# Kernel tuning notes

Hardware: AMD Instinct MI355X
Metric: run time of the kernel (lower is better)

The kernel has to match this reference:

```python
import jax, jax.numpy as jnp
import numpy as np

# dims
B, N, T, F, D = 16, 64, 168, 8, 248   # batch, stations, seq, features, gcn_dim
E = D + F                              # transformer dmodel = 256
H = 8                                  # attention heads
FF = 4 * E                             # expansion_factor * dmodel


def _layer_norm(x, g, b, eps=1e-5):
    m = jnp.mean(x, axis=-1, keepdims=True)
    v = jnp.var(x, axis=-1, keepdims=True)
    return (x - m) * jax.lax.rsqrt(v + eps) * g + b


def setup_inputs() -> dict:
    key = jax.random.key(0)
    ks = jax.random.split(key, 20)
    s = 0.02
    return {
        'x': jax.random.normal(ks[0], (B, N, T, F), jnp.float32),
        'locs': jax.random.uniform(ks[1], (B, N, 2), jnp.float32),
        'pos_em': jax.random.normal(ks[2], (B, T, E), jnp.float32),
        'periodic_em': jax.random.normal(ks[3], (B, T, E), jnp.float32),
        'gcn_w': jax.random.normal(ks[4], (F, D), jnp.float32) * s,
        'gcn_b': jnp.zeros((D,), jnp.float32),
        'fc1_w': jax.random.normal(ks[5], (D, D), jnp.float32) * s,
        'fc1_b': jnp.zeros((D,), jnp.float32),
        'wq': jax.random.normal(ks[6], (E, E), jnp.float32) * s,
        'bq': jnp.zeros((E,), jnp.float32),
        'wk': jax.random.normal(ks[7], (E, E), jnp.float32) * s,
        'bk': jnp.zeros((E,), jnp.float32),
        'wv': jax.random.normal(ks[8], (E, E), jnp.float32) * s,
        'bv': jnp.zeros((E,), jnp.float32),
        'wo': jax.random.normal(ks[9], (E, E), jnp.float32) * s,
        'bo': jnp.zeros((E,), jnp.float32),
        'ln1_g': jnp.ones((E,), jnp.float32),
        'ln1_b': jnp.zeros((E,), jnp.float32),
        'ln2_g': jnp.ones((E,), jnp.float32),
        'ln2_b': jnp.zeros((E,), jnp.float32),
        'ff1_w': jax.random.normal(ks[10], (E, FF), jnp.float32) * s,
        'ff1_b': jnp.zeros((FF,), jnp.float32),
        'ff2_w': jax.random.normal(ks[11], (FF, E), jnp.float32) * s,
        'ff2_b': jnp.zeros((E,), jnp.float32),
    }


def reference(x, locs, pos_em, periodic_em, gcn_w, gcn_b, fc1_w, fc1_b,
              wq, bq, wk, bk, wv, bv, wo, bo,
              ln1_g, ln1_b, ln2_g, ln2_b, ff1_w, ff1_b, ff2_w, ff2_b):
    b, n, t, f = x.shape
    # --- inverse-distance-weighted dense adjacency (fully connected graph) ---
    diff = locs[:, :, None, :] - locs[:, None, :, :]            # [B,N,N,2]
    dist = jnp.sqrt(jnp.sum(diff * diff, -1) + 1e-12)           # [B,N,N]
    w = jnp.where(jnp.eye(n, dtype=bool), 0.0, 1.0 / dist)      # no self edges
    w = w / jnp.sum(w, -1, keepdims=True)                       # norm=True
    # --- GCNConv (self loops + symmetric normalization), batched over B and T ---
    a = w + jnp.eye(n, dtype=x.dtype)
    dinv = jax.lax.rsqrt(jnp.sum(a, -1))
    a = a * dinv[:, :, None] * dinv[:, None, :]                 # [B,N,N]
    h = jnp.einsum('bntf,fd->bntd', x, gcn_w)                   # xW
    g = jax.nn.relu(jnp.einsum('bmn,bntd->bmtd', a, h) + gcn_b) # aggregate + relu
    g = jnp.einsum('bntd,de->bnte', g, fc1_w) + fc1_b           # fc1
    # --- concat features, flatten stations into batch, add positional embedding ---
    tok = jnp.concatenate([x, g], -1).reshape(b * n, t, -1)     # [B*N,T,E]
    tok = tok + jnp.repeat(pos_em, n, axis=0)                   # dropout=identity (eval)
    per = jnp.repeat(periodic_em, n, axis=0)
    # --- transformer encoder layer (periodic embedding conditions Q/K) ---
    e = tok.shape[-1]
    dh = e // H
    qk_in = tok + per
    q = (qk_in @ wq + bq).reshape(b * n, t, H, dh)
    k = (qk_in @ wk + bk).reshape(b * n, t, H, dh)
    v = (tok @ wv + bv).reshape(b * n, t, H, dh)
    s = jnp.einsum('bthd,bshd->bhts', q, k) * (1.0 / float(np.sqrt(dh)))
    p = jax.nn.softmax(s, axis=-1)
    o = jnp.einsum('bhts,bshd->bthd', p, v).reshape(b * n, t, e)
    o = o @ wo + bo
    h1 = _layer_norm(tok + o, ln1_g, ln1_b)
    ff = jax.nn.relu(h1 @ ff1_w + ff1_b) @ ff2_w + ff2_b
    out = _layer_norm(h1 + ff, ln2_g, ln2_b)
    return out.reshape(b, n, t, e)
```

## Files before the change

kernel.cpp:

```cpp
#include <hip/hip_runtime.h>
#include <hip/hip_bf16.h>

constexpr int B_  = 16;
constexpr int N_  = 64;
constexpr int T_  = 168;
constexpr int F_  = 8;
constexpr int E_  = 256;
constexpr int H_  = 8;
constexpr int DH_ = 32;
constexpr int NT_ = N_ * T_;
constexpr int LDQ_ = 768;

typedef __bf16 bf16x8 __attribute__((ext_vector_type(8)));
typedef float  f32x4  __attribute__((ext_vector_type(4)));
typedef float  f32x4u __attribute__((ext_vector_type(4), aligned(4)));

__device__ __forceinline__ unsigned short f2b(float f) {
  union { float f; unsigned int u; } v; v.f = f;
  unsigned int r = (v.u + 0x7FFFu + ((v.u >> 16) & 1u)) >> 16;
  return (unsigned short)r;
}
__device__ __forceinline__ float b2f(unsigned short h) {
  union { unsigned int u; float f; } v; v.u = ((unsigned int)h) << 16;
  return v.f;
}
__device__ __forceinline__ unsigned int cvtpk(float lo, float hi) {
  unsigned int r;
  asm("v_cvt_pk_bf16_f32 %0, %1, %2" : "=v"(r) : "v"(lo), "v"(hi));
  return r;
}
__device__ __forceinline__ void gload16(const void* g, void* l) {
  __builtin_amdgcn_global_load_lds(
      (const __attribute__((address_space(1))) unsigned int*)g,
      (__attribute__((address_space(3))) unsigned int*)l, 16, 0, 0);
}

__global__ void adj_kernel(const float* __restrict__ locs, float* __restrict__ a) {
  int b = blockIdx.x;
  int m = threadIdx.x;
  __shared__ float lx[64], ly[64];
  lx[m] = locs[(b * 64 + m) * 2 + 0];
  ly[m] = locs[(b * 64 + m) * 2 + 1];
  __syncthreads();
  float x = lx[m], y = ly[m];
  float sum = 0.f;
  for (int n = 0; n < 64; ++n) {
    float dx = x - lx[n], dy = y - ly[n];
    float d = sqrtf(dx * dx + dy * dy + 1e-12f);
    sum += (n == m) ? 0.f : 1.f / d;
  }
  float inv = 0.5f / sum;
  for (int n = 0; n < 64; ++n) {
    float dx = x - lx[n], dy = y - ly[n];
    float d = sqrtf(dx * dx + dy * dy + 1e-12f);
    float w = (n == m) ? 0.5f : inv / d;
    a[(b * 64 + m) * 64 + n] = w;
  }
}

__global__ void convw_kernel(const float* __restrict__ in, unsigned short* __restrict__ outT,
                             int K, int N, int Kp, int Np) {
  int idx = blockIdx.x * 256 + threadIdx.x;
  if (idx >= Np * Kp) return;
  int n = idx / Kp, k = idx % Kp;
  float v = (k < K && n < N) ? in[(long)k * N + n] : 0.f;
  outT[idx] = f2b(v);
}

__global__ __launch_bounds__(256) void gcn_kernel(
    const float* __restrict__ x, const float* __restrict__ adj,
    const float* __restrict__ gcn_w, const float* __restrict__ gcn_b,
    const float* __restrict__ pos_em, const float* __restrict__ per_em,
    unsigned short* __restrict__ G, unsigned short* __restrict__ tokb,
    unsigned short* __restrict__ qkb, int b0) {
  int bl = blockIdx.x / T_;
  int t = blockIdx.x % T_;
  int b = b0 + bl;
  int tid = threadIdx.x;
  __shared__ float sX[512];
  __shared__ float sXA[512];
  const float* adjb = adj + b * 4096;
  for (int i = tid; i < 512; i += 256) {
    int n = i >> 3, f = i & 7;
    sX[i] = x[((long)(b * 64 + n) * T_ + t) * F_ + f];
  }
  __syncthreads();
  for (int i = tid; i < 512; i += 256) {
    int m = i >> 3, f = i & 7;
    float s = 0.f;
    for (int n = 0; n < 64; ++n) s += adjb[(m << 6) + n] * sX[(n << 3) + f];
    sXA[i] = s;
  }
  {
    long pbase = ((long)bl * T_ + t) * E_;
    for (int i = tid; i < 512; i += 256) {
      int m = i >> 3, f = i & 7;
      long lrow = (long)(bl * 64 + m) * T_ + t;
      float base = sX[i] + pos_em[pbase + f];
      tokb[lrow * E_ + f] = f2b(base);
      qkb[lrow * E_ + f]  = f2b(base + per_em[pbase + f]);
    }
  }
  __syncthreads();
  for (int i = tid; i < 64 * 256; i += 256) {
    int m = i >> 8, d = i & 255;
    float v = 0.f;
    if (d < 248) {
      float s = gcn_b[d];
      const float* xam = &sXA[m << 3];
#pragma unroll
      for (int f = 0; f < 8; ++f) s += xam[f] * gcn_w[f * 248 + d];
      v = fmaxf(s, 0.f);
    }
    long lrow = (long)(bl * 64 + m) * T_ + t;
    G[lrow * 256 + d] = f2b(v);
  }
}

template <int KCHUNKS, int WAVES>
__global__ __launch_bounds__(WAVES * 64) void block_gemm(
    const unsigned short* __restrict__ A, int lda,
    const unsigned short* __restrict__ Bt, int K, int Nact,
    const float* __restrict__ bias,
    float* Cf, unsigned short* Cb1, unsigned short* Cb2,
    const float* __restrict__ emb1, const float* __restrict__ emb2,
    const unsigned short* __restrict__ resb, const float* resf,
    int c0, int ldc, int relu) {
  __shared__ unsigned short As[64 * 256];
  const int tid = threadIdx.x;
  const int lane = tid & 63, w = tid >> 6;
  const int l15 = lane & 15, lg = lane >> 4;
  const int m0 = blockIdx.x * 64;
  const int n0w = blockIdx.y * (WAVES * 64) + w * 64;

  f32x4 acc[4][4];
#pragma unroll
  for (int i = 0; i < 4; ++i)
#pragma unroll
    for (int j = 0; j < 4; ++j) acc[i][j] = (f32x4){0.f, 0.f, 0.f, 0.f};

  for (int kc = 0; kc < KCHUNKS; ++kc) {
    if (kc) __syncthreads();
#pragma unroll
    for (int j = 0; j < 32 / WAVES; ++j) {
      int idx = j * (WAVES * 64) + tid;
      int row = idx >> 5, g = idx & 31;
      int swg = (g & 24) | ((g & 7) ^ (row & 7));
      gload16(A + (long)(m0 + row) * lda + kc * 256 + swg * 8,
              &As[(j * (WAVES * 64) + w * 64) * 8]);
    }
    bf16x8 Wa[4], Wb[4], Xf[4];
    auto ldw = [&](bf16x8 (&W)[4], int ks) {
#pragma unroll
      for (int nf = 0; nf < 4; ++nf)
        W[nf] = *reinterpret_cast<const bf16x8*>(
            Bt + (long)(n0w + nf * 16 + l15) * K + kc * 256 + ks * 32 + (lg << 3));
    };
    auto ldx = [&](int ks) {
#pragma unroll
      for (int mf = 0; mf < 4; ++mf) {
        int row = (mf << 4) + l15;
        int ksg = (ks << 2) + lg;
        int sw = (ksg & 24) | ((ksg & 7) ^ (row & 7));
        Xf[mf] = *reinterpret_cast<const bf16x8*>(&As[((row << 5) + sw) * 8]);
      }
    };
    auto mm = [&](bf16x8 (&W)[4]) {
#pragma unroll
      for (int mf = 0; mf < 4; ++mf)
#pragma unroll
        for (int nf = 0; nf < 4; ++nf)
          acc[mf][nf] = __builtin_amdgcn_mfma_f32_16x16x32_bf16(W[nf], Xf[mf], acc[mf][nf], 0, 0, 0);
    };
    ldw(Wa, 0);
    asm volatile("s_waitcnt vmcnt(0)" ::: "memory");
    __syncthreads();
#pragma unroll
    for (int kp = 0; kp < 4; ++kp) {
      ldw(Wb, kp * 2 + 1);
      ldx(kp * 2);
      mm(Wa);
      if (kp < 3) ldw(Wa, kp * 2 + 2);
      ldx(kp * 2 + 1);
      mm(Wb);
    }
  }

  const int cb = lg << 2;
#pragma unroll
  for (int mf = 0; mf < 4; ++mf) {
    int rr = m0 + (mf << 4) + l15;
    int ar = (rr / NT_) * T_ + (rr % T_);
    long rbase  = (long)rr * ldc + c0;
    long rbase2 = (long)rr * 256 + c0;
    long abase  = (long)ar * 256 + c0;
#pragma unroll
    for (int nf = 0; nf < 4; ++nf) {
      int gcol = n0w + (nf << 4) + cb;
      if (gcol < Nact) {
        float v0 = acc[mf][nf][0], v1 = acc[mf][nf][1];
        float v2 = acc[mf][nf][2], v3 = acc[mf][nf][3];
        if (bias) {
          f32x4u b4 = *reinterpret_cast<const f32x4u*>(bias + gcol);
          v0 += b4[0]; v1 += b4[1]; v2 += b4[2]; v3 += b4[3];
        }
        if (relu) {
          v0 = fmaxf(v0, 0.f); v1 = fmaxf(v1, 0.f);
          v2 = fmaxf(v2, 0.f); v3 = fmaxf(v3, 0.f);
        }
        if (resb) {
          ushort4 rv = *reinterpret_cast<const ushort4*>(resb + rbase2 + gcol);
          v0 += b2f(rv.x); v1 += b2f(rv.y); v2 += b2f(rv.z); v3 += b2f(rv.w);
        }
        if (resf) {
          f32x4u r4 = *reinterpret_cast<const f32x4u*>(resf + rbase + gcol);
          v0 += r4[0]; v1 += r4[1]; v2 += r4[2]; v3 += r4[3];
        }
        if (emb1) {
          f32x4u e4 = *reinterpret_cast<const f32x4u*>(emb1 + abase + gcol);
          v0 += e4[0]; v1 += e4[1]; v2 += e4[2]; v3 += e4[3];
        }
        if (Cf) {
          f32x4u o; o[0] = v0; o[1] = v1; o[2] = v2; o[3] = v3;
          *reinterpret_cast<f32x4u*>(Cf + rbase + gcol) = o;
        }
        if (Cb1) {
          uint2 p = {cvtpk(v0, v1), cvtpk(v2, v3)};
          *reinterpret_cast<uint2*>(Cb1 + rbase + gcol) = p;
        }
        if (Cb2) {
          f32x4u e4 = *reinterpret_cast<const f32x4u*>(emb2 + abase + gcol);
          uint2 p = {cvtpk(v0 + e4[0], v1 + e4[1]), cvtpk(v2 + e4[2], v3 + e4[3])};
          *reinterpret_cast<uint2*>(Cb2 + rbase + gcol) = p;
        }
      }
    }
  }
}

__global__ __launch_bounds__(256) void wo_ln_kernel(
    const unsigned short* __restrict__ A, int lda,
    const unsigned short* __restrict__ Wt,
    const float* __restrict__ bias,
    const unsigned short* __restrict__ resb,
    const float* __restrict__ lng, const float* __restrict__ lnb,
    unsigned short* __restrict__ outb) {
  __shared__ unsigned short As[64 * 256];
  __shared__ float red[4][4][16][2];
  const int tid = threadIdx.x;
  const int lane = tid & 63, w = tid >> 6;
  const int l15 = lane & 15, lg = lane >> 4;
  const int m0 = blockIdx.x * 64;
  const int n0w = w * 64;

  f32x4 acc[4][4];
#pragma unroll
  for (int i = 0; i < 4; ++i)
#pragma unroll
    for (int j = 0; j < 4; ++j) acc[i][j] = (f32x4){0.f, 0.f, 0.f, 0.f};

#pragma unroll
  for (int j = 0; j < 8; ++j) {
    int idx = j * 256 + tid;
    int row = idx >> 5, g = idx & 31;
    int swg = (g & 24) | ((g & 7) ^ (row & 7));
    gload16(A + (long)(m0 + row) * lda + swg * 8, &As[(j * 256 + w * 64) * 8]);
  }
  bf16x8 Wa[4], Wb[4], Xf[4];
  auto ldw = [&](bf16x8 (&W)[4], int ks) {
#pragma unroll
    for (int nf = 0; nf < 4; ++nf)
      W[nf] = *reinterpret_cast<const bf16x8*>(
          Wt + (long)(n0w + nf * 16 + l15) * 256 + ks * 32 + (lg << 3));
  };
  auto ldx = [&](int ks) {
#pragma unroll
    for (int mf = 0; mf < 4; ++mf) {
      int row = (mf << 4) + l15;
      int ksg = (ks << 2) + lg;
      int sw = (ksg & 24) | ((ksg & 7) ^ (row & 7));
      Xf[mf] = *reinterpret_cast<const bf16x8*>(&As[((row << 5) + sw) * 8]);
    }
  };
  auto mm = [&](bf16x8 (&W)[4]) {
#pragma unroll
    for (int mf = 0; mf < 4; ++mf)
#pragma unroll
      for (int nf = 0; nf < 4; ++nf)
        acc[mf][nf] = __builtin_amdgcn_mfma_f32_16x16x32_bf16(W[nf], Xf[mf], acc[mf][nf], 0, 0, 0);
  };
  ldw(Wa, 0);
  asm volatile("s_waitcnt vmcnt(0)" ::: "memory");
  __syncthreads();
#pragma unroll
  for (int kp = 0; kp < 4; ++kp) {
    ldw(Wb, kp * 2 + 1);
    ldx(kp * 2);
    mm(Wa);
    if (kp < 3) ldw(Wa, kp * 2 + 2);
    ldx(kp * 2 + 1);
    mm(Wb);
  }

  const int cb = lg << 2;
  float s[4], s2[4];
#pragma unroll
  for (int mf = 0; mf < 4; ++mf) {
    int rr = m0 + (mf << 4) + l15;
    long rbase2 = (long)rr * 256;
    s[mf] = 0.f; s2[mf] = 0.f;
#pragma unroll
    for (int nf = 0; nf < 4; ++nf) {
      int gcol = n0w + (nf << 4) + cb;
      f32x4u b4 = *reinterpret_cast<const f32x4u*>(bias + gcol);
      ushort4 rv = *reinterpret_cast<const ushort4*>(resb + rbase2 + gcol);
      float v0 = acc[mf][nf][0] + b4[0] + b2f(rv.x);
      float v1 = acc[mf][nf][1] + b4[1] + b2f(rv.y);
      float v2 = acc[mf][nf][2] + b4[2] + b2f(rv.z);
      float v3 = acc[mf][nf][3] + b4[3] + b2f(rv.w);
      acc[mf][nf][0] = v0; acc[mf][nf][1] = v1;
      acc[mf][nf][2] = v2; acc[mf][nf][3] = v3;
      s[mf] += v0 + v1 + v2 + v3;
      s2[mf] += v0 * v0 + v1 * v1 + v2 * v2 + v3 * v3;
    }
    s[mf] += __shfl_xor(s[mf], 16, 64);
    s[mf] += __shfl_xor(s[mf], 32, 64);
    s2[mf] += __shfl_xor(s2[mf], 16, 64);
    s2[mf] += __shfl_xor(s2[mf], 32, 64);
    if (lg == 0) { red[w][mf][l15][0] = s[mf]; red[w][mf][l15][1] = s2[mf]; }
  }
  __syncthreads();
#pragma unroll
  for (int mf = 0; mf < 4; ++mf) {
    float S  = red[0][mf][l15][0] + red[1][mf][l15][0] + red[2][mf][l15][0] + red[3][mf][l15][0];
    float S2 = red[0][mf][l15][1] + red[1][mf][l15][1] + red[2][mf][l15][1] + red[3][mf][l15][1];
    float mean = S * 0.00390625f;
    float var = S2 * 0.00390625f - mean * mean;
    float rs = rsqrtf(var + 1e-5f);
    int rr = m0 + (mf << 4) + l15;
    long rbase = (long)rr * 256;
#pragma unroll
    for (int nf = 0; nf < 4; ++nf) {
      int gcol = n0w + (nf << 4) + cb;
      f32x4u g4 = *reinterpret_cast<const f32x4u*>(lng + gcol);
      f32x4u t4 = *reinterpret_cast<const f32x4u*>(lnb + gcol);
      float o0 = (acc[mf][nf][0] - mean) * rs * g4[0] + t4[0];
      float o1 = (acc[mf][nf][1] - mean) * rs * g4[1] + t4[1];
      float o2 = (acc[mf][nf][2] - mean) * rs * g4[2] + t4[2];
      float o3 = (acc[mf][nf][3] - mean) * rs * g4[3] + t4[3];
      uint2 p = {cvtpk(o0, o1), cvtpk(o2, o3)};
      *reinterpret_cast<uint2*>(outb + rbase + gcol) = p;
    }
  }
}

__global__ __launch_bounds__(256) void ff_fused_kernel(
    const unsigned short* __restrict__ h1,
    const unsigned short* __restrict__ W1,
    const unsigned short* __restrict__ W2,
    const float* __restrict__ b1, const float* __restrict__ b2,
    const float* __restrict__ lng, const float* __restrict__ lnb,
    float* __restrict__ out) {
  __shared__ unsigned short h1s[64 * 256];
  __shared__ unsigned short fis[64 * 128];
  __shared__ float red[4][4][16][2];
  const int tid = threadIdx.x;
  const int lane = tid & 63, w = tid >> 6;
  const int l15 = lane & 15, lg = lane >> 4;
  const int m0 = blockIdx.x * 64;

#pragma unroll
  for (int j = 0; j < 8; ++j) {
    int idx = j * 256 + tid;
    int row = idx >> 5, g = idx & 31;
    int swg = (g & 24) | ((g & 7) ^ (row & 7));
    gload16(h1 + (long)(m0 + row) * 256 + swg * 8, &h1s[(j * 256 + w * 64) * 8]);
  }

  f32x4 acc2[4][4];
#pragma unroll
  for (int i = 0; i < 4; ++i)
#pragma unroll
    for (int j = 0; j < 4; ++j) acc2[i][j] = (f32x4){0.f, 0.f, 0.f, 0.f};

  bf16x8 W1a[2], W1b[2], Wa[4], Wb[4], Xf[4];
  auto ldw1 = [&](bf16x8 (&W)[2], int hc, int ks) {
#pragma unroll
    for (int nf = 0; nf < 2; ++nf)
      W[nf] = *reinterpret_cast<const bf16x8*>(
          W1 + (long)(hc * 128 + w * 32 + nf * 16 + l15) * 256 + ks * 32 + (lg << 3));
  };
  auto ldw2 = [&](bf16x8 (&W)[4], int hc, int ks) {
#pragma unroll
    for (int nf = 0; nf < 4; ++nf)
      W[nf] = *reinterpret_cast<const bf16x8*>(
          W2 + (long)(w * 64 + nf * 16 + l15) * 1024 + hc * 128 + ks * 32 + (lg << 3));
  };
  auto ldxh = [&](int ks) {
#pragma unroll
    for (int mf = 0; mf < 4; ++mf) {
      int row = (mf << 4) + l15;
      int ksg = (ks << 2) + lg;
      int sw = (ksg & 24) | ((ksg & 7) ^ (row & 7));
      Xf[mf] = *reinterpret_cast<const bf16x8*>(&h1s[((row << 5) + sw) * 8]);
    }
  };
  auto ldxf = [&](int ks) {
#pragma unroll
    for (int mf = 0; mf < 4; ++mf) {
      int row = (mf << 4) + l15;
      int ksg = (ks << 2) + lg;
      int sw = (ksg & 8) | ((ksg & 7) ^ (row & 7));
      Xf[mf] = *reinterpret_cast<const bf16x8*>(&fis[((row << 4) + sw) * 8]);
    }
  };

  const int cb = lg << 2;
  bool first = true;
  for (int hc = 0; hc < 8; ++hc) {
    f32x4 acc1[4][2];
#pragma unroll
    for (int i = 0; i < 4; ++i)
#pragma unroll
      for (int j = 0; j < 2; ++j) acc1[i][j] = (f32x4){0.f, 0.f, 0.f, 0.f};
    ldw1(W1a, hc, 0);
    if (first) {
      asm volatile("s_waitcnt vmcnt(2)" ::: "memory");
      __syncthreads();
      first = false;
    }
#pragma unroll
    for (int kp = 0; kp < 4; ++kp) {
      ldw1(W1b, hc, kp * 2 + 1);
      ldxh(kp * 2);
#pragma unroll
      for (int mf = 0; mf < 4; ++mf)
#pragma unroll
        for (int nf = 0; nf < 2; ++nf)
          acc1[mf][nf] = __builtin_amdgcn_mfma_f32_16x16x32_bf16(W1a[nf], Xf[mf], acc1[mf][nf], 0, 0, 0);
      if (kp < 3) ldw1(W1a, hc, kp * 2 + 2);
      ldxh(kp * 2 + 1);
#pragma unroll
      for (int mf = 0; mf < 4; ++mf)
#pragma unroll
        for (int nf = 0; nf < 2; ++nf)
          acc1[mf][nf] = __builtin_amdgcn_mfma_f32_16x16x32_bf16(W1b[nf], Xf[mf], acc1[mf][nf], 0, 0, 0);
    }
    if (hc) __syncthreads();
#pragma unroll
    for (int mf = 0; mf < 4; ++mf) {
      int row = (mf << 4) + l15;
#pragma unroll
      for (int nf = 0; nf < 2; ++nf) {
        int col = w * 32 + (nf << 4) + cb;
        f32x4u b4 = *reinterpret_cast<const f32x4u*>(b1 + hc * 128 + col);
        float v0 = fmaxf(acc1[mf][nf][0] + b4[0], 0.f);
        float v1 = fmaxf(acc1[mf][nf][1] + b4[1], 0.f);
        float v2 = fmaxf(acc1[mf][nf][2] + b4[2], 0.f);
        float v3 = fmaxf(acc1[mf][nf][3] + b4[3], 0.f);
        int g = col >> 3;
        int swg = (g & 8) | ((g & 7) ^ (row & 7));
        uint2 p = {cvtpk(v0, v1), cvtpk(v2, v3)};
        *reinterpret_cast<uint2*>(&fis[((row << 4) + swg) * 8 + (col & 7)]) = p;
      }
    }
    ldw2(Wa, hc, 0);
    __syncthreads();
#pragma unroll
    for (int kp = 0; kp < 2; ++kp) {
      ldw2(Wb, hc, kp * 2 + 1);
      ldxf(kp * 2);
#pragma unroll
      for (int mf = 0; mf < 4; ++mf)
#pragma unroll
        for (int nf = 0; nf < 4; ++nf)
          acc2[mf][nf] = __builtin_amdgcn_mfma_f32_16x16x32_bf16(Wa[nf], Xf[mf], acc2[mf][nf], 0, 0, 0);
      if (kp < 1) ldw2(Wa, hc, kp * 2 + 2);
      ldxf(kp * 2 + 1);
#pragma unroll
      for (int mf = 0; mf < 4; ++mf)
#pragma unroll
        for (int nf = 0; nf < 4; ++nf)
          acc2[mf][nf] = __builtin_amdgcn_mfma_f32_16x16x32_bf16(Wb[nf], Xf[mf], acc2[mf][nf], 0, 0, 0);
    }
  }

  float s[4], s2[4];
#pragma unroll
  for (int mf = 0; mf < 4; ++mf) {
    int row = (mf << 4) + l15;
    s[mf] = 0.f; s2[mf] = 0.f;
#pragma unroll
    for (int nf = 0; nf < 4; ++nf) {
      int gcol = w * 64 + (nf << 4) + cb;
      f32x4u b4 = *reinterpret_cast<const f32x4u*>(b2 + gcol);
      int g = gcol >> 3;
      int swg = (g & 24) | ((g & 7) ^ (row & 7));
      ushort4 rv = *reinterpret_cast<const ushort4*>(&h1s[((row << 5) + swg) * 8 + (gcol & 7)]);
      float v0 = acc2[mf][nf][0] + b4[0] + b2f(rv.x);
      float v1 = acc2[mf][nf][1] + b4[1] + b2f(rv.y);
      float v2 = acc2[mf][nf][2] + b4[2] + b2f(rv.z);
      float v3 = acc2[mf][nf][3] + b4[3] + b2f(rv.w);
      acc2[mf][nf][0] = v0; acc2[mf][nf][1] = v1;
      acc2[mf][nf][2] = v2; acc2[mf][nf][3] = v3;
      s[mf] += v0 + v1 + v2 + v3;
      s2[mf] += v0 * v0 + v1 * v1 + v2 * v2 + v3 * v3;
    }
    s[mf] += __shfl_xor(s[mf], 16, 64);
    s[mf] += __shfl_xor(s[mf], 32, 64);
    s2[mf] += __shfl_xor(s2[mf], 16, 64);
    s2[mf] += __shfl_xor(s2[mf], 32, 64);
    if (lg == 0) { red[w][mf][l15][0] = s[mf]; red[w][mf][l15][1] = s2[mf]; }
  }
  __syncthreads();
#pragma unroll
  for (int mf = 0; mf < 4; ++mf) {
    float S  = red[0][mf][l15][0] + red[1][mf][l15][0] + red[2][mf][l15][0] + red[3][mf][l15][0];
    float S2 = red[0][mf][l15][1] + red[1][mf][l15][1] + red[2][mf][l15][1] + red[3][mf][l15][1];
    float mean = S * 0.00390625f;
    float var = S2 * 0.00390625f - mean * mean;
    float rs = rsqrtf(var + 1e-5f);
    int rr = m0 + (mf << 4) + l15;
    long rbase = (long)rr * 256;
#pragma unroll
    for (int nf = 0; nf < 4; ++nf) {
      int gcol = w * 64 + (nf << 4) + cb;
      f32x4u g4 = *reinterpret_cast<const f32x4u*>(lng + gcol);
      f32x4u t4 = *reinterpret_cast<const f32x4u*>(lnb + gcol);
      f32x4u o;
      o[0] = (acc2[mf][nf][0] - mean) * rs * g4[0] + t4[0];
      o[1] = (acc2[mf][nf][1] - mean) * rs * g4[1] + t4[1];
      o[2] = (acc2[mf][nf][2] - mean) * rs * g4[2] + t4[2];
      o[3] = (acc2[mf][nf][3] - mean) * rs * g4[3] + t4[3];
      *reinterpret_cast<f32x4u*>(out + rbase + gcol) = o;
    }
  }
}

__global__ __launch_bounds__(256) void attn_mfma_kernel(unsigned short* QKV) {
  int blk = blockIdx.x;
  int bn = blk >> 3, h = blk & 7;
  int tid = threadIdx.x;
  int lane = tid & 63, w = tid >> 6;

  __shared__ unsigned short Kfr[11 * 512];
  __shared__ unsigned short VT[32][200];
  __shared__ unsigned short Pb[4][16][200];

  const long qbase = (long)bn * T_ * LDQ_ + h * DH_;
  const unsigned short* Kg = QKV + qbase + 256;
  const unsigned short* V  = QKV + qbase + 512;
  const unsigned short* Q  = QKV + qbase;
  unsigned short* O = QKV + qbase;
  int l15 = lane & 15, lg = lane >> 4;

  for (int kt = w; kt < 11; kt += 4) {
    gload16(Kg + (long)(kt * 16 + l15) * LDQ_ + (lg << 3), &Kfr[kt * 512]);
  }
  for (int i = tid; i < T_ * 4; i += 256) {
    int t = i >> 2, seg = (i & 3) << 3;
    uint4 vv = *reinterpret_cast<const uint4*>(V + (long)t * LDQ_ + seg);
    const unsigned short* vs = (const unsigned short*)&vv;
#pragma unroll
    for (int j = 0; j < 8; ++j) VT[seg + j][t] = vs[j];
  }
  for (int i = tid; i < 32 * 32; i += 256) VT[i >> 5][168 + (i & 31)] = 0;
  {
    unsigned short* pflat = &Pb[0][0][0];
    for (int i = tid; i < 64 * 24; i += 256)
      pflat[(i / 24) * 200 + 176 + (i % 24)] = 0;
  }
  __syncthreads();

  const float scale = 0.17677669529663687f;
  unsigned short* Pw = &Pb[w][0][0];

  for (int it = 0; it < 3; ++it) {
    int qt = w + it * 4;
    if (qt > 10) break;
    bf16x8 af = *reinterpret_cast<const bf16x8*>(
        Q + (long)(qt * 16 + l15) * LDQ_ + (lg << 3));
    f32x4 s[11];
#pragma unroll
    for (int kt = 0; kt < 11; ++kt) {
      bf16x8 bf = *reinterpret_cast<const bf16x8*>(&Kfr[kt * 512 + lane * 8]);
      s[kt] = __builtin_amdgcn_mfma_f32_16x16x32_bf16(
          af, bf, (f32x4){0.f, 0.f, 0.f, 0.f}, 0, 0, 0);
    }
    bool ok10 = (l15 < 8);
    float inv_l[4];
#pragma unroll
    for (int r = 0; r < 4; ++r) {
      float mx = -1e30f;
#pragma unroll
      for (int kt = 0; kt < 10; ++kt) mx = fmaxf(mx, s[kt][r] * scale);
      if (ok10) mx = fmaxf(mx, s[10][r] * scale);
#pragma unroll
      for (int off = 1; off < 16; off <<= 1) mx = fmaxf(mx, __shfl_xor(mx, off, 64));
      float pv[11];
      float ls = 0.f;
#pragma unroll
      for (int kt = 0; kt < 11; ++kt) {
        bool valid = (kt < 10) || ok10;
        float p = valid ? __expf(s[kt][r] * scale - mx) : 0.f;
        pv[kt] = p;
        ls += p;
      }
#pragma unroll
      for (int off = 1; off < 16; off <<= 1) ls += __shfl_xor(ls, off, 64);
      inv_l[r] = 1.f / ls;
      int prow = (lg << 2) + r;
#pragma unroll
      for (int kt = 0; kt < 11; ++kt)
        Pw[prow * 200 + kt * 16 + l15] = f2b(pv[kt]);
    }
    asm volatile("s_waitcnt lgkmcnt(0)" ::: "memory");
    __builtin_amdgcn_sched_barrier(0);
    f32x4 o0 = (f32x4){0.f, 0.f, 0.f, 0.f};
    f32x4 o1 = (f32x4){0.f, 0.f, 0.f, 0.f};
#pragma unroll
    for (int ks = 0; ks < 6; ++ks) {
      bf16x8 pf = *reinterpret_cast<const bf16x8*>(&Pw[l15 * 200 + ks * 32 + (lg << 3)]);
      bf16x8 v0 = *reinterpret_cast<const bf16x8*>(&VT[l15][ks * 32 + (lg << 3)]);
      bf16x8 v1 = *reinterpret_cast<const bf16x8*>(&VT[16 + l15][ks * 32 + (lg << 3)]);
      o0 = __builtin_amdgcn_mfma_f32_16x16x32_bf16(pf, v0, o0, 0, 0, 0);
      o1 = __builtin_amdgcn_mfma_f32_16x16x32_bf16(pf, v1, o1, 0, 0, 0);
    }
    int rg = lg << 2;
#pragma unroll
    for (int r = 0; r < 4; ++r) {
      int q = qt * 16 + rg + r;
      if (q < T_) {
        long ob = (long)q * LDQ_;
        O[ob + l15]      = f2b(o0[r] * inv_l[r]);
        O[ob + 16 + l15] = f2b(o1[r] * inv_l[r]);
      }
    }
  }
}

extern "C" void kernel_launch(void* const* d_in, const int* in_sizes, int n_in,
                              void* d_out, int out_size, void* d_ws, size_t ws_size,
                              hipStream_t stream) {
  const float* x      = (const float*)d_in[0];
  const float* locs   = (const float*)d_in[1];
  const float* pos_em = (const float*)d_in[2];
  const float* per_em = (const float*)d_in[3];
  const float* gcn_w  = (const float*)d_in[4];
  const float* gcn_b  = (const float*)d_in[5];
  const float* fc1_w  = (const float*)d_in[6];
  const float* fc1_b  = (const float*)d_in[7];
  const float* wq = (const float*)d_in[8];
  const float* bq = (const float*)d_in[9];
  const float* wk = (const float*)d_in[10];
  const float* bk = (const float*)d_in[11];
  const float* wv = (const float*)d_in[12];
  const float* bv = (const float*)d_in[13];
  const float* wo = (const float*)d_in[14];
  const float* bo = (const float*)d_in[15];
  const float* ln1_g = (const float*)d_in[16];
  const float* ln1_b = (const float*)d_in[17];
  const float* ln2_g = (const float*)d_in[18];
  const float* ln2_b = (const float*)d_in[19];
  const float* ff1_w = (const float*)d_in[20];
  const float* ff1_b = (const float*)d_in[21];
  const float* ff2_w = (const float*)d_in[22];
  const float* ff2_b = (const float*)d_in[23];
  float* out = (float*)d_out;

  const size_t ADJ_BYTES = 1u << 20;
  const size_t WB_BYTES  = 2u << 20;
  int CB = 16;
  while (CB > 1) {
    if (ADJ_BYTES + WB_BYTES + (size_t)CB * NT_ * 2560 <= ws_size) break;
    CB >>= 1;
  }
  char* ws = (char*)d_ws;
  float* adj = (float*)ws;
  unsigned short* wslab = (unsigned short*)(ws + ADJ_BYTES);
  unsigned short* fc1T  = wslab;
  unsigned short* wqkT  = wslab + 65536;
  unsigned short* wkT   = wslab + 2 * 65536;
  unsigned short* wvT   = wslab + 3 * 65536;
  unsigned short* woT   = wslab + 4 * 65536;
  unsigned short* ff1T  = wslab + 5 * 65536;
  unsigned short* ff2T  = wslab + 5 * 65536 + 262144;
  float* bqk = (float*)(ws + ADJ_BYTES + 1900544);

  unsigned short* tokb = (unsigned short*)(ws + ADJ_BYTES + WB_BYTES);
  unsigned short* qkb  = tokb + (size_t)CB * NT_ * 256;
  unsigned short* qkv  = qkb + (size_t)CB * NT_ * 256;
  unsigned short* h1b  = tokb;

  adj_kernel<<<B_, 64, 0, stream>>>(locs, adj);
  convw_kernel<<<256, 256, 0, stream>>>(fc1_w, fc1T, 248, 248, 256, 256);
  convw_kernel<<<256, 256, 0, stream>>>(wq, wqkT, 256, 256, 256, 256);
  convw_kernel<<<256, 256, 0, stream>>>(wk, wkT, 256, 256, 256, 256);
  convw_kernel<<<256, 256, 0, stream>>>(wv, wvT, 256, 256, 256, 256);
  convw_kernel<<<256, 256, 0, stream>>>(wo, woT, 256, 256, 256, 256);
  convw_kernel<<<1024, 256, 0, stream>>>(ff1_w, ff1T, 256, 1024, 256, 1024);
  convw_kernel<<<1024, 256, 0, stream>>>(ff2_w, ff2T, 1024, 256, 1024, 256);
  hipMemcpyAsync(bqk, bq, 256 * sizeof(float), hipMemcpyDeviceToDevice, stream);
  hipMemcpyAsync(bqk + 256, bk, 256 * sizeof(float), hipMemcpyDeviceToDevice, stream);

  for (int b0 = 0; b0 < B_; b0 += CB) {
    const int rows = CB * NT_;
    const int GX = rows / 64;
    const float* pos_c = pos_em + (long)b0 * T_ * E_;
    const float* per_c = per_em + (long)b0 * T_ * E_;
    float* out_c = out + (long)b0 * NT_ * E_;
    unsigned short* G = qkv;

    gcn_kernel<<<CB * T_, 256, 0, stream>>>(x, adj, gcn_w, gcn_b, pos_c, per_c,
                                            G, tokb, qkb, b0);
    block_gemm<1, 4><<<dim3(GX, 1), 256, 0, stream>>>(
        G, 256, fc1T, 256, 248, fc1_b, nullptr, tokb, qkb, pos_c, per_c,
        nullptr, nullptr, 8, 256, 0);
    block_gemm<1, 8><<<dim3(GX, 1), 512, 0, stream>>>(
        qkb, 256, wqkT, 256, 512, bqk, nullptr, qkv, nullptr, nullptr, nullptr,
        nullptr, nullptr, 0, LDQ_, 0);
    block_gemm<1, 4><<<dim3(GX, 1), 256, 0, stream>>>(
        tokb, 256, wvT, 256, 256, bv, nullptr, qkv, nullptr, nullptr, nullptr,
        nullptr, nullptr, 512, LDQ_, 0);
    attn_mfma_kernel<<<CB * N_ * H_, 256, 0, stream>>>(qkv);
    wo_ln_kernel<<<GX, 256, 0, stream>>>(qkv, LDQ_, woT, bo, tokb,
                                         ln1_g, ln1_b, h1b);
    ff_fused_kernel<<<GX, 256, 0, stream>>>(h1b, ff1T, ff2T, ff1_b, ff2_b,
                                            ln2_g, ln2_b, out_c);
  }
}
```

Measured before the change: 1.153 ms.

## Split fused FFN kernel across 8 waves and raise MFMA issue priority

The fused FFN kernel now runs with 512 threads (8 waves) per 64-row block instead of 4, so each wave owns half as many output columns in both GEMMs. This cuts per-wave accumulator registers and gives more waves to hide load latency. The LayerNorm reduction buffer and loops are widened to cover 8 waves. s_setprio around the MFMA bursts is also added here and in the other GEMM kernels, to favour matrix issue over loads. The trade-off is more block barriers and more redundant LDS fragment reads per block.

```diff
diff --git a/kernel.cpp b/kernel.cpp
--- a/kernel.cpp
+++ b/kernel.cpp
@@ -166,11 +166,13 @@
       }
     };
     auto mm = [&](bf16x8 (&W)[4]) {
+      __builtin_amdgcn_s_setprio(1);
 #pragma unroll
       for (int mf = 0; mf < 4; ++mf)
 #pragma unroll
         for (int nf = 0; nf < 4; ++nf)
           acc[mf][nf] = __builtin_amdgcn_mfma_f32_16x16x32_bf16(W[nf], Xf[mf], acc[mf][nf], 0, 0, 0);
+      __builtin_amdgcn_s_setprio(0);
     };
     ldw(Wa, 0);
     asm volatile("s_waitcnt vmcnt(0)" ::: "memory");
@@ -283,11 +285,13 @@
     }
   };
   auto mm = [&](bf16x8 (&W)[4]) {
+    __builtin_amdgcn_s_setprio(1);
 #pragma unroll
     for (int mf = 0; mf < 4; ++mf)
 #pragma unroll
       for (int nf = 0; nf < 4; ++nf)
         acc[mf][nf] = __builtin_amdgcn_mfma_f32_16x16x32_bf16(W[nf], Xf[mf], acc[mf][nf], 0, 0, 0);
+    __builtin_amdgcn_s_setprio(0);
   };
   ldw(Wa, 0);
   asm volatile("s_waitcnt vmcnt(0)" ::: "memory");
@@ -354,7 +358,7 @@
   }
 }
 
-__global__ __launch_bounds__(256) void ff_fused_kernel(
+__global__ __launch_bounds__(512, 4) void ff_fused_kernel(
     const unsigned short* __restrict__ h1,
     const unsigned short* __restrict__ W1,
     const unsigned short* __restrict__ W2,
@@ -363,38 +367,36 @@
     float* __restrict__ out) {
   __shared__ unsigned short h1s[64 * 256];
   __shared__ unsigned short fis[64 * 128];
-  __shared__ float red[4][4][16][2];
+  __shared__ float red[8][4][16][2];
   const int tid = threadIdx.x;
   const int lane = tid & 63, w = tid >> 6;
   const int l15 = lane & 15, lg = lane >> 4;
   const int m0 = blockIdx.x * 64;
 
 #pragma unroll
-  for (int j = 0; j < 8; ++j) {
-    int idx = j * 256 + tid;
+  for (int j = 0; j < 4; ++j) {
+    int idx = j * 512 + tid;
     int row = idx >> 5, g = idx & 31;
     int swg = (g & 24) | ((g & 7) ^ (row & 7));
-    gload16(h1 + (long)(m0 + row) * 256 + swg * 8, &h1s[(j * 256 + w * 64) * 8]);
-  }
-
-  f32x4 acc2[4][4];
+    gload16(h1 + (long)(m0 + row) * 256 + swg * 8, &h1s[(j * 512 + w * 64) * 8]);
+  }
+
+  f32x4 acc2[4][2];
 #pragma unroll
   for (int i = 0; i < 4; ++i)
 #pragma unroll
-    for (int j = 0; j < 4; ++j) acc2[i][j] = (f32x4){0.f, 0.f, 0.f, 0.f};
-
-  bf16x8 W1a[2], W1b[2], Wa[4], Wb[4], Xf[4];
-  auto ldw1 = [&](bf16x8 (&W)[2], int hc, int ks) {
+    for (int j = 0; j < 2; ++j) acc2[i][j] = (f32x4){0.f, 0.f, 0.f, 0.f};
+
+  bf16x8 W1a, W1b, W2a[2], W2b[2], Xf[4];
+  auto ldw1 = [&](bf16x8& W, int hc, int ks) {
+    W = *reinterpret_cast<const bf16x8*>(
+        W1 + (long)(hc * 128 + w * 16 + l15) * 256 + ks * 32 + (lg << 3));
+  };
+  auto ldw2 = [&](bf16x8 (&W)[2], int hc, int ks) {
 #pragma unroll
     for (int nf = 0; nf < 2; ++nf)
       W[nf] = *reinterpret_cast<const bf16x8*>(
-          W1 + (long)(hc * 128 + w * 32 + nf * 16 + l15) * 256 + ks * 32 + (lg << 3));
-  };
-  auto ldw2 = [&](bf16x8 (&W)[4], int hc, int ks) {
-#pragma unroll
-    for (int nf = 0; nf < 4; ++nf)
-      W[nf] = *reinterpret_cast<const bf16x8*>(
-          W2 + (long)(w * 64 + nf * 16 + l15) * 1024 + hc * 128 + ks * 32 + (lg << 3));
+          W2 + (long)(w * 32 + nf * 16 + l15) * 1024 + hc * 128 + ks * 32 + (lg << 3));
   };
   auto ldxh = [&](int ks) {
 #pragma unroll
@@ -418,14 +420,12 @@
   const int cb = lg << 2;
   bool first = true;
   for (int hc = 0; hc < 8; ++hc) {
-    f32x4 acc1[4][2];
-#pragma unroll
-    for (int i = 0; i < 4; ++i)
-#pragma unroll
-      for (int j = 0; j < 2; ++j) acc1[i][j] = (f32x4){0.f, 0.f, 0.f, 0.f};
+    f32x4 acc1[4];
+#pragma unroll
+    for (int i = 0; i < 4; ++i) acc1[i] = (f32x4){0.f, 0.f, 0.f, 0.f};
     ldw1(W1a, hc, 0);
     if (first) {
-      asm volatile("s_waitcnt vmcnt(2)" ::: "memory");
+      asm volatile("s_waitcnt vmcnt(1)" ::: "memory");
       __syncthreads();
       first = false;
     }
@@ -433,55 +433,56 @@
     for (int kp = 0; kp < 4; ++kp) {
       ldw1(W1b, hc, kp * 2 + 1);
       ldxh(kp * 2);
+      __builtin_amdgcn_s_setprio(1);
 #pragma unroll
       for (int mf = 0; mf < 4; ++mf)
-#pragma unroll
-        for (int nf = 0; nf < 2; ++nf)
-          acc1[mf][nf] = __builtin_amdgcn_mfma_f32_16x16x32_bf16(W1a[nf], Xf[mf], acc1[mf][nf], 0, 0, 0);
+        acc1[mf] = __builtin_amdgcn_mfma_f32_16x16x32_bf16(W1a, Xf[mf], acc1[mf], 0, 0, 0);
+      __builtin_amdgcn_s_setprio(0);
       if (kp < 3) ldw1(W1a, hc, kp * 2 + 2);
       ldxh(kp * 2 + 1);
+      __builtin_amdgcn_s_setprio(1);
 #pragma unroll
       for (int mf = 0; mf < 4; ++mf)
-#pragma unroll
-        for (int nf = 0; nf < 2; ++nf)
-          acc1[mf][nf] = __builtin_amdgcn_mfma_f32_16x16x32_bf16(W1b[nf], Xf[mf], acc1[mf][nf], 0, 0, 0);
+        acc1[mf] = __builtin_amdgcn_mfma_f32_16x16x32_bf16(W1b, Xf[mf], acc1[mf], 0, 0, 0);
+      __builtin_amdgcn_s_setprio(0);
     }
     if (hc) __syncthreads();
 #pragma unroll
     for (int mf = 0; mf < 4; ++mf) {
       int row = (mf << 4) + l15;
-#pragma unroll
-      for (int nf = 0; nf < 2; ++nf) {
-        int col = w * 32 + (nf << 4) + cb;
-        f32x4u b4 = *reinterpret_cast<const f32x4u*>(b1 + hc * 128 + col);
-        float v0 = fmaxf(acc1[mf][nf][0] + b4[0], 0.f);
-        float v1 = fmaxf(acc1[mf][nf][1] + b4[1], 0.f);
-        float v2 = fmaxf(acc1[mf][nf][2] + b4[2], 0.f);
-        float v3 = fmaxf(acc1[mf][nf][3] + b4[3], 0.f);
-        int g = col >> 3;
-        int swg = (g & 8) | ((g & 7) ^ (row & 7));
-        uint2 p = {cvtpk(v0, v1), cvtpk(v2, v3)};
-        *reinterpret_cast<uint2*>(&fis[((row << 4) + swg) * 8 + (col & 7)]) = p;
-      }
-    }
-    ldw2(Wa, hc, 0);
+      int col = w * 16 + cb;
+      f32x4u b4 = *reinterpret_cast<const f32x4u*>(b1 + hc * 128 + col);
+      float v0 = fmaxf(acc1[mf][0] + b4[0], 0.f);
+      float v1 = fmaxf(acc1[mf][1] + b4[1], 0.f);
+      float v2 = fmaxf(acc1[mf][2] + b4[2], 0.f);
+      float v3 = fmaxf(acc1[mf][3] + b4[3], 0.f);
+      int g = col >> 3;
+      int swg = (g & 8) | ((g & 7) ^ (row & 7));
+      uint2 p = {cvtpk(v0, v1), cvtpk(v2, v3)};
+      *reinterpret_cast<uint2*>(&fis[((row << 4) + swg) * 8 + (col & 7)]) = p;
+    }
+    ldw2(W2a, hc, 0);
     __syncthreads();
 #pragma unroll
     for (int kp = 0; kp < 2; ++kp) {
-      ldw2(Wb, hc, kp * 2 + 1);
+      ldw2(W2b, hc, kp * 2 + 1);
       ldxf(kp * 2);
+      __builtin_amdgcn_s_setprio(1);
 #pragma unroll
       for (int mf = 0; mf < 4; ++mf)
 #pragma unroll
-        for (int nf = 0; nf < 4; ++nf)
-          acc2[mf][nf] = __builtin_amdgcn_mfma_f32_16x16x32_bf16(Wa[nf], Xf[mf], acc2[mf][nf], 0, 0, 0);
-      if (kp < 1) ldw2(Wa, hc, kp * 2 + 2);
+        for (int nf = 0; nf < 2; ++nf)
+          acc2[mf][nf] = __builtin_amdgcn_mfma_f32_16x16x32_bf16(W2a[nf], Xf[mf], acc2[mf][nf], 0, 0, 0);
+      __builtin_amdgcn_s_setprio(0);
+      if (kp < 1) ldw2(W2a, hc, kp * 2 + 2);
       ldxf(kp * 2 + 1);
+      __builtin_amdgcn_s_setprio(1);
 #pragma unroll
       for (int mf = 0; mf < 4; ++mf)
 #pragma unroll
-        for (int nf = 0; nf < 4; ++nf)
-          acc2[mf][nf] = __builtin_amdgcn_mfma_f32_16x16x32_bf16(Wb[nf], Xf[mf], acc2[mf][nf], 0, 0, 0);
+        for (int nf = 0; nf < 2; ++nf)
+          acc2[mf][nf] = __builtin_amdgcn_mfma_f32_16x16x32_bf16(W2b[nf], Xf[mf], acc2[mf][nf], 0, 0, 0);
+      __builtin_amdgcn_s_setprio(0);
     }
   }
 
@@ -491,8 +492,8 @@
     int row = (mf << 4) + l15;
     s[mf] = 0.f; s2[mf] = 0.f;
 #pragma unroll
-    for (int nf = 0; nf < 4; ++nf) {
-      int gcol = w * 64 + (nf << 4) + cb;
+    for (int nf = 0; nf < 2; ++nf) {
+      int gcol = w * 32 + (nf << 4) + cb;
       f32x4u b4 = *reinterpret_cast<const f32x4u*>(b2 + gcol);
       int g = gcol >> 3;
       int swg = (g & 24) | ((g & 7) ^ (row & 7));
@@ -515,16 +516,17 @@
   __syncthreads();
 #pragma unroll
   for (int mf = 0; mf < 4; ++mf) {
-    float S  = red[0][mf][l15][0] + red[1][mf][l15][0] + red[2][mf][l15][0] + red[3][mf][l15][0];
-    float S2 = red[0][mf][l15][1] + red[1][mf][l15][1] + red[2][mf][l15][1] + red[3][mf][l15][1];
+    float S = 0.f, S2 = 0.f;
+#pragma unroll
+    for (int ww = 0; ww < 8; ++ww) { S += red[ww][mf][l15][0]; S2 += red[ww][mf][l15][1]; }
     float mean = S * 0.00390625f;
     float var = S2 * 0.00390625f - mean * mean;
     float rs = rsqrtf(var + 1e-5f);
     int rr = m0 + (mf << 4) + l15;
     long rbase = (long)rr * 256;
 #pragma unroll
-    for (int nf = 0; nf < 4; ++nf) {
-      int gcol = w * 64 + (nf << 4) + cb;
+    for (int nf = 0; nf < 2; ++nf) {
+      int gcol = w * 32 + (nf << 4) + cb;
       f32x4u g4 = *reinterpret_cast<const f32x4u*>(lng + gcol);
       f32x4u t4 = *reinterpret_cast<const f32x4u*>(lnb + gcol);
       f32x4u o;
@@ -725,7 +727,7 @@
     attn_mfma_kernel<<<CB * N_ * H_, 256, 0, stream>>>(qkv);
     wo_ln_kernel<<<GX, 256, 0, stream>>>(qkv, LDQ_, woT, bo, tokb,
                                          ln1_g, ln1_b, h1b);
-    ff_fused_kernel<<<GX, 256, 0, stream>>>(h1b, ff1T, ff2T, ff1_b, ff2_b,
+    ff_fused_kernel<<<GX, 512, 0, stream>>>(h1b, ff1T, ff2T, ff1_b, ff2_b,
                                             ln2_g, ln2_b, out_c);
   }
 }
```

New measurement: 1.153 ms (median of 2 runs). No clear change (+0.0%).
